# Performance work log

Measured on AMD Instinct MI355X. Metric: run time of the kernel, lower is better.

## Reference

```python
import jax, jax.numpy as jnp
import numpy as np

B, S, D, H = 2, 2048, 1024, 16
HD = D // H  # head_dim = 64


def _rope(t, cos, sin):
    # t: (B, H, S, HD); cos/sin: (S, HD//2) -> rotate interleaved pairs
    t2 = t.reshape(*t.shape[:-1], HD // 2, 2)
    t1, t2_ = t2[..., 0], t2[..., 1]
    c = cos[None, None, :, :]
    s = sin[None, None, :, :]
    out = jnp.stack([t1 * c - t2_ * s, t1 * s + t2_ * c], axis=-1)
    return out.reshape(t.shape)


def setup_inputs() -> dict:
    key = jax.random.key(0)
    ks = jax.random.split(key, 5)
    x = jax.random.normal(ks[0], (B, S, D), dtype=jnp.float32)
    attn_mask = jnp.tril(jnp.ones((S, S), dtype=bool))  # causal
    # standard RoPE angles: pos * inv_freq
    inv_freq = 1.0 / (10000.0 ** (jnp.arange(0, HD, 2, dtype=jnp.float32) / HD))
    freqs = jnp.arange(S, dtype=jnp.float32)[:, None] * inv_freq[None, :]  # (S, HD//2)
    std = 1.0 / np.sqrt(D)
    w_qkv = jax.random.normal(ks[1], (3 * D, D), dtype=jnp.float32) * std
    b_qkv = jnp.zeros((3 * D,), dtype=jnp.float32)
    w_proj = jax.random.normal(ks[2], (D, D), dtype=jnp.float32) * std
    b_proj = jnp.zeros((D,), dtype=jnp.float32)
    return {"x": x, "attn_mask": attn_mask, "freqs": freqs,
            "w_qkv": w_qkv, "b_qkv": b_qkv, "w_proj": w_proj, "b_proj": b_proj}


def reference(x, attn_mask, freqs, w_qkv, b_qkv, w_proj, b_proj):
    # QKV projection: (B,S,D) -> (B,S,3D), split per einops pattern (three, H, HD)
    qkv = x @ w_qkv.T + b_qkv
    qkv = qkv.reshape(B, S, 3, H, HD)
    q = jnp.transpose(qkv[:, :, 0], (0, 2, 1, 3))  # (B,H,S,HD)
    k = jnp.transpose(qkv[:, :, 1], (0, 2, 1, 3))
    v = jnp.transpose(qkv[:, :, 2], (0, 2, 1, 3))
    cos, sin = jnp.cos(freqs), jnp.sin(freqs)
    q = _rope(q, cos, sin)
    k = _rope(k, cos, sin)
    scale = 1.0 / np.sqrt(HD)
    scores = jnp.einsum("bhqd,bhkd->bhqk", q, k) * scale  # (B,H,S,S)
    scores = jnp.where(attn_mask[None, None, :, :], scores, jnp.finfo(scores.dtype).min)
    attn = jax.nn.softmax(scores, axis=-1)
    out = jnp.einsum("bhqk,bhkd->bhqd", attn, v)  # (B,H,S,HD)
    out = jnp.transpose(out, (0, 2, 1, 3)).reshape(B, S, D)
    return out @ w_proj.T + b_proj
```

## Files before the change

### kernel.cpp

```cpp
#include <hip/hip_runtime.h>

#define S_LEN 2048
#define NH 16
#define HD 64
#define DMODEL 1024

typedef __bf16 bf16x8 __attribute__((ext_vector_type(8)));
typedef float floatx4 __attribute__((ext_vector_type(4)));
typedef short short8 __attribute__((ext_vector_type(8)));

__device__ inline unsigned short f2bf(float f) {
    union { float f; unsigned u; } v; v.f = f;
    unsigned u = v.u;
    unsigned r = (u + 0x7FFFu + ((u >> 16) & 1u)) >> 16;
    return (unsigned short)r;
}

__device__ __forceinline__ void gload_lds16(const void* g, void* l) {
    __builtin_amdgcn_global_load_lds(
        (const __attribute__((address_space(1))) unsigned int*)g,
        (__attribute__((address_space(3))) unsigned int*)l, 16, 0, 0);
}

__device__ __forceinline__ void cvt4(const float4* __restrict__ src,
                                     uint2* __restrict__ dst, int i) {
    float4 v = src[i];
    union { unsigned short u[4]; uint2 d; } o;
    o.u[0] = f2bf(v.x); o.u[1] = f2bf(v.y); o.u[2] = f2bf(v.z); o.u[3] = f2bf(v.w);
    dst[i] = o.d;
}

__global__ __launch_bounds__(256) void prep_kernel(
    const float* __restrict__ x, const float* __restrict__ wq,
    const float* __restrict__ wp, const float* __restrict__ freqs,
    unsigned short* __restrict__ xb, unsigned short* __restrict__ wqb,
    unsigned short* __restrict__ wpb, float2* __restrict__ cs)
{
    const int tid = blockIdx.x * 256 + threadIdx.x;
    const int nth = gridDim.x * 256;
    for (int i = tid; i < (4096 * 1024) / 4; i += nth) cvt4((const float4*)x, (uint2*)xb, i);
    for (int i = tid; i < (3072 * 1024) / 4; i += nth) cvt4((const float4*)wq, (uint2*)wqb, i);
    for (int i = tid; i < (1024 * 1024) / 4; i += nth) cvt4((const float4*)wp, (uint2*)wpb, i);
    for (int i = tid; i < S_LEN * 32; i += nth) {
        const float f = freqs[i];
        float2 c; c.x = cosf(f); c.y = sinf(f);
        cs[i] = c;
    }
}

#define SROW(r) (((r) & 3) ^ (((r) >> 2) & 3))

#define QKV_STAGE(dA, dB, kk) do { \
    gload_lds16(ag + (kk),               (dA) + wv * 512); \
    gload_lds16(ag + 64 * DMODEL + (kk), (dA) + 2048 + wv * 512); \
    gload_lds16(bg + (kk),               (dB) + wv * 512); \
    gload_lds16(bg + 64 * DMODEL + (kk), (dB) + 2048 + wv * 512); \
} while (0)

#define QKV_COMPUTE(sA, sB) do { \
    bf16x8 af[4]; \
    _Pragma("unroll") for (int m_ = 0; m_ < 4; m_++) af[m_] = *(const bf16x8*)&(sA)[aoff[m_]]; \
    _Pragma("unroll") for (int n_ = 0; n_ < 4; n_++) { \
        bf16x8 bf = *(const bf16x8*)&(sB)[boff[n_]]; \
        _Pragma("unroll") for (int m_ = 0; m_ < 4; m_++) \
            acc[m_][n_] = __builtin_amdgcn_mfma_f32_16x16x32_bf16(af[m_], bf, acc[m_][n_], 0, 0, 0); \
    } \
} while (0)

__global__ __launch_bounds__(256, 3) void qkv_gemm_kernel(
    const unsigned short* __restrict__ xb, const unsigned short* __restrict__ wqb,
    const float* __restrict__ bias, const float2* __restrict__ cs,
    unsigned short* __restrict__ qb, unsigned short* __restrict__ kb,
    unsigned short* __restrict__ vb)
{
    __shared__ __align__(16) unsigned short smem[16384];
    unsigned short* A0 = smem;
    unsigned short* B0 = smem + 4096;
    unsigned short* A1 = smem + 8192;
    unsigned short* B1 = smem + 12288;

    const int t = threadIdx.x;
    const int v = (blockIdx.x & 7) * 96 + (blockIdx.x >> 3);
    const int mbase = (v / 24) * 128;
    const int nbase = (v % 24) * 128;
    const int wv = t >> 6, lane = t & 63;
    const int quad = lane >> 4, l16 = lane & 15;
    const int wr = wv >> 1, wc = wv & 1;

    floatx4 acc[4][4];
    #pragma unroll
    for (int m = 0; m < 4; m++)
        #pragma unroll
        for (int n = 0; n < 4; n++)
            #pragma unroll
            for (int r = 0; r < 4; r++) acc[m][n][r] = 0.f;

    const int srow = t >> 2;
    const int schunk = (t & 3) ^ SROW(srow);
    const unsigned short* ag = xb + (size_t)(mbase + srow) * DMODEL + schunk * 8;
    const unsigned short* bg = wqb + (size_t)(nbase + srow) * DMODEL + schunk * 8;

    const int Sl = SROW(l16);
    int aoff[4], boff[4];
    #pragma unroll
    for (int m = 0; m < 4; m++) aoff[m] = (wr * 64 + m * 16 + l16) * 32 + (quad ^ Sl) * 8;
    #pragma unroll
    for (int n = 0; n < 4; n++) boff[n] = (wc * 64 + n * 16 + l16) * 32 + (quad ^ Sl) * 8;

    QKV_STAGE(A0, B0, 0);
    __syncthreads();
    for (int k0 = 0; k0 < DMODEL; k0 += 64) {
        QKV_STAGE(A1, B1, k0 + 32);
        QKV_COMPUTE(A0, B0);
        __syncthreads();
        if (k0 + 64 < DMODEL) QKV_STAGE(A0, B0, k0 + 64);
        QKV_COMPUTE(A1, B1);
        __syncthreads();
    }

    const int part = nbase >> 10;
    const int bidx = mbase >> 11;
    const int s0   = mbase & 2047;

    if (part == 2) {
        unsigned short* Vt = smem;
        const int hb = (nbase & 1023) >> 6;
        float bvv[4];
        #pragma unroll
        for (int nt = 0; nt < 4; nt++) bvv[nt] = bias[nbase + wc * 64 + nt * 16 + l16];
        #pragma unroll
        for (int shalf = 0; shalf < 2; shalf++) {
            __syncthreads();
            if (wr == shalf) {
                #pragma unroll
                for (int nt = 0; nt < 4; nt++) {
                    const int hdl = wc * 64 + nt * 16 + l16;
                    #pragma unroll
                    for (int m = 0; m < 4; m++)
                        #pragma unroll
                        for (int r = 0; r < 4; r++)
                            Vt[hdl * 72 + m * 16 + quad * 4 + r] = f2bf(acc[m][nt][r] + bvv[nt]);
                }
            }
            __syncthreads();
            const int hdl = t & 127, sp = t >> 7;
            const size_t bh2 = (size_t)bidx * NH + hb + (hdl >> 6);
            #pragma unroll
            for (int c = 0; c < 4; c++) {
                const int sl0 = (sp * 4 + c) * 8;
                const int sg = s0 + shalf * 64 + sl0;
                short8 vv = *(const short8*)&Vt[hdl * 72 + sl0];
                *(short8*)&vb[((bh2 * 256 + (sg >> 3)) * 64 + (hdl & 63)) * 8] = vv;
            }
        }
    } else {
        const size_t bhb = (size_t)bidx * NH;
        const int odd = l16 & 1;
        #pragma unroll
        for (int nt = 0; nt < 4; nt++) {
            const int n_ = nbase + wc * 64 + nt * 16 + l16;
            const int hd = n_ & 63;
            const size_t bh = bhb + ((n_ & 1023) >> 6);
            const float bvv = bias[n_];
            const int ci = (nt * 16 + l16) >> 1;
            #pragma unroll
            for (int m = 0; m < 4; m++) {
                #pragma unroll
                for (int r = 0; r < 4; r++) {
                    const int s = s0 + wr * 64 + m * 16 + quad * 4 + r;
                    float val = acc[m][nt][r] + bvv;
                    float other = __shfl_xor(val, 1, 64);
                    const float2 csv = cs[(size_t)s * 32 + ci];
                    float outv = odd ? fmaf(other, csv.y, val * csv.x)
                                     : fmaf(-other, csv.y, val * csv.x);
                    if (part == 0) {
                        qb[(bh * S_LEN + s) * HD + hd] = f2bf(outv * 0.125f);
                    } else {
                        kb[((bh * 8 + (hd >> 3)) * (size_t)S_LEN + s) * 8 + (hd & 7)] = f2bf(outv);
                    }
                }
            }
        }
    }
}

__global__ __launch_bounds__(256, 4) void attn_kernel(
    const unsigned short* __restrict__ qb, const unsigned short* __restrict__ kb,
    const unsigned short* __restrict__ vbk, unsigned short* __restrict__ ao)
{
    __shared__ __align__(16) unsigned short Ks[8 * 512];
    __shared__ __align__(16) unsigned short Vt[8 * 512];
    __shared__ __align__(16) unsigned short Pw[4][16 * 72];

    const int t = threadIdx.x;
    const int wv = t >> 6, lane = t & 63, quad = lane >> 4, l16 = lane & 15;
    const int qt   = blockIdx.x >> 5;
    const int bhid = blockIdx.x & 31;
    const int h = bhid & 15, b = bhid >> 4;
    const size_t bh = (size_t)b * NH + h;
    const unsigned short* qg  = qb + bh * S_LEN * HD;
    const unsigned short* kgB = kb + bh * 8 * S_LEN * 8;
    const unsigned short* vgB = vbk + bh * 256 * 64 * 8;

    bf16x8 qf[2];
    {
        const unsigned short* q0 = qg + (size_t)(qt * 64 + wv * 16 + l16) * HD;
        qf[0] = *(const bf16x8*)&q0[quad * 8];
        qf[1] = *(const bf16x8*)&q0[32 + quad * 8];
    }

    bf16x8 ones;
    {
        union { short8 s; bf16x8 v; } o;
        for (int j = 0; j < 8; j++) o.s[j] = 0x3F80;
        ones = o.v;
    }

    floatx4 lfr = {0.f, 0.f, 0.f, 0.f};
    floatx4 Ofr[4];
    for (int nt = 0; nt < 4; nt++)
        for (int r = 0; r < 4; r++) Ofr[nt][r] = 0.f;

    const int ntiles = qt + 1;

    for (int kt = 0; kt < ntiles; kt++) {
        const int kbase = kt * 64;
        {
            const unsigned short* g0 = kgB + ((size_t)(2 * wv) * S_LEN + kbase + lane) * 8;
            gload_lds16(g0,             &Ks[(2 * wv) * 512]);
            gload_lds16(g0 + S_LEN * 8, &Ks[(2 * wv + 1) * 512]);
            const unsigned short* g1 = vgB + ((size_t)((kbase >> 3) + 2 * wv) * 64 + lane) * 8;
            gload_lds16(g1,          &Vt[(2 * wv) * 512]);
            gload_lds16(g1 + 64 * 8, &Vt[(2 * wv + 1) * 512]);
        }
        __syncthreads();

        float pex[4][4];
        #pragma unroll
        for (int sub = 0; sub < 4; sub++) {
            bf16x8 kf0 = *(const bf16x8*)&Ks[(0 * 4 + quad) * 512 + (sub * 16 + l16) * 8];
            bf16x8 kf1 = *(const bf16x8*)&Ks[(1 * 4 + quad) * 512 + (sub * 16 + l16) * 8];
            floatx4 sacc = {0.f, 0.f, 0.f, 0.f};
            sacc = __builtin_amdgcn_mfma_f32_16x16x32_bf16(kf0, qf[0], sacc, 0, 0, 0);
            sacc = __builtin_amdgcn_mfma_f32_16x16x32_bf16(kf1, qf[1], sacc, 0, 0, 0);
            #pragma unroll
            for (int r = 0; r < 4; r++) pex[sub][r] = sacc[r];
        }
        if (kt == qt) {
            const int q = qt * 64 + wv * 16 + l16;
            #pragma unroll
            for (int sub = 0; sub < 4; sub++)
                #pragma unroll
                for (int r = 0; r < 4; r++) {
                    const int key = kbase + sub * 16 + quad * 4 + r;
                    if (key > q) pex[sub][r] = -1e30f;
                }
        }
        #pragma unroll
        for (int sub = 0; sub < 4; sub++) {
            union { unsigned short s[4]; uint2 u; } pk;
            #pragma unroll
            for (int r = 0; r < 4; r++) pk.s[r] = f2bf(__expf(pex[sub][r]));
            *(uint2*)&Pw[wv][l16 * 72 + sub * 16 + quad * 4] = pk.u;
        }
        bf16x8 pf0 = *(const bf16x8*)&Pw[wv][l16 * 72 + quad * 8];
        bf16x8 pf1 = *(const bf16x8*)&Pw[wv][l16 * 72 + 32 + quad * 8];
        lfr = __builtin_amdgcn_mfma_f32_16x16x32_bf16(ones, pf0, lfr, 0, 0, 0);
        lfr = __builtin_amdgcn_mfma_f32_16x16x32_bf16(ones, pf1, lfr, 0, 0, 0);
        #pragma unroll
        for (int nt = 0; nt < 4; nt++) {
            bf16x8 v0 = *(const bf16x8*)&Vt[(0 * 4 + quad) * 512 + (nt * 16 + l16) * 8];
            bf16x8 v1 = *(const bf16x8*)&Vt[(1 * 4 + quad) * 512 + (nt * 16 + l16) * 8];
            Ofr[nt] = __builtin_amdgcn_mfma_f32_16x16x32_bf16(pf0, v0, Ofr[nt], 0, 0, 0);
            Ofr[nt] = __builtin_amdgcn_mfma_f32_16x16x32_bf16(pf1, v1, Ofr[nt], 0, 0, 0);
        }
        __syncthreads();
    }

    float linv[4];
    #pragma unroll
    for (int r = 0; r < 4; r++) {
        float lq = __shfl(lfr[0], (lane & 48) | (quad * 4 + r), 64);
        linv[r] = 1.f / lq;
    }
    #pragma unroll
    for (int nt = 0; nt < 4; nt++)
        #pragma unroll
        for (int r = 0; r < 4; r++) {
            const int s = qt * 64 + wv * 16 + quad * 4 + r;
            ao[((size_t)b * S_LEN + s) * DMODEL + h * HD + nt * 16 + l16] =
                f2bf(Ofr[nt][r] * linv[r]);
        }
}

#define PROJ_STAGE(dA, dB, kk) do { \
    gload_lds16(ag + (kk),               (dA) + wv * 512); \
    gload_lds16(ag + 64 * DMODEL + (kk), (dA) + 2048 + wv * 512); \
    gload_lds16(bg + (kk),               (dB) + wv * 512); \
} while (0)

#define PROJ_COMPUTE(sA, sB) do { \
    bf16x8 af[4]; \
    _Pragma("unroll") for (int m_ = 0; m_ < 4; m_++) af[m_] = *(const bf16x8*)&(sA)[aoff[m_]]; \
    _Pragma("unroll") for (int n_ = 0; n_ < 2; n_++) { \
        bf16x8 bf = *(const bf16x8*)&(sB)[boff[n_]]; \
        _Pragma("unroll") for (int m_ = 0; m_ < 4; m_++) \
            acc[m_][n_] = __builtin_amdgcn_mfma_f32_16x16x32_bf16(af[m_], bf, acc[m_][n_], 0, 0, 0); \
    } \
} while (0)

__global__ __launch_bounds__(256, 3) void proj_kernel(
    const unsigned short* __restrict__ a, const unsigned short* __restrict__ wpb,
    const float* __restrict__ bias, float* __restrict__ out)
{
    __shared__ __align__(16) unsigned short smem[12288];
    unsigned short* A0 = smem;
    unsigned short* B0 = smem + 4096;
    unsigned short* A1 = smem + 6144;
    unsigned short* B1 = smem + 10240;

    const int t = threadIdx.x;
    const int v = (blockIdx.x & 7) * 64 + (blockIdx.x >> 3);
    const int mbase = (v >> 4) * 128;
    const int nbase = (v & 15) * 64;
    const int wv = t >> 6, lane = t & 63, quad = lane >> 4, l16 = lane & 15;
    const int wr = wv >> 1, wc = wv & 1;

    floatx4 acc[4][2];
    #pragma unroll
    for (int m = 0; m < 4; m++)
        #pragma unroll
        for (int n = 0; n < 2; n++)
            #pragma unroll
            for (int r = 0; r < 4; r++) acc[m][n][r] = 0.f;

    const int srow = t >> 2;
    const int schunk = (t & 3) ^ SROW(srow);
    const unsigned short* ag = a + (size_t)(mbase + srow) * DMODEL + schunk * 8;
    const unsigned short* bg = wpb + (size_t)(nbase + srow) * DMODEL + schunk * 8;

    const int Sl = SROW(l16);
    int aoff[4], boff[2];
    #pragma unroll
    for (int m = 0; m < 4; m++) aoff[m] = (wr * 64 + m * 16 + l16) * 32 + (quad ^ Sl) * 8;
    #pragma unroll
    for (int n = 0; n < 2; n++) boff[n] = (wc * 32 + n * 16 + l16) * 32 + (quad ^ Sl) * 8;

    PROJ_STAGE(A0, B0, 0);
    __syncthreads();
    for (int k0 = 0; k0 < DMODEL; k0 += 64) {
        PROJ_STAGE(A1, B1, k0 + 32);
        PROJ_COMPUTE(A0, B0);
        __syncthreads();
        if (k0 + 64 < DMODEL) PROJ_STAGE(A0, B0, k0 + 64);
        PROJ_COMPUTE(A1, B1);
        __syncthreads();
    }

    #pragma unroll
    for (int n = 0; n < 2; n++) {
        const int nn = nbase + wc * 32 + n * 16 + l16;
        const float bvv = bias[nn];
        #pragma unroll
        for (int m = 0; m < 4; m++)
            #pragma unroll
            for (int r = 0; r < 4; r++)
                out[(size_t)(mbase + wr * 64 + m * 16 + quad * 4 + r) * DMODEL + nn] =
                    acc[m][n][r] + bvv;
    }
}

extern "C" void kernel_launch(void* const* d_in, const int* in_sizes, int n_in,
                              void* d_out, int out_size, void* d_ws, size_t ws_size,
                              hipStream_t stream) {
    const float* x      = (const float*)d_in[0];
    const float* freqs  = (const float*)d_in[2];
    const float* w_qkv  = (const float*)d_in[3];
    const float* b_qkv  = (const float*)d_in[4];
    const float* w_proj = (const float*)d_in[5];
    const float* b_proj = (const float*)d_in[6];
    float* out = (float*)d_out;

    unsigned short* ws = (unsigned short*)d_ws;
    const size_t HSZ = (size_t)2 * NH * S_LEN * HD;
    unsigned short* qb  = ws;
    unsigned short* kb  = ws + HSZ;
    unsigned short* vb  = ws + 2 * HSZ;
    unsigned short* ao  = ws + 3 * HSZ;
    unsigned short* xb  = ws + 4 * HSZ;
    unsigned short* wqb = xb + (size_t)4096 * 1024;
    unsigned short* wpb = wqb + (size_t)3072 * 1024;
    float2* cs = (float2*)(wpb + (size_t)1024 * 1024);

    prep_kernel<<<2048, 256, 0, stream>>>(x, w_qkv, w_proj, freqs, xb, wqb, wpb, cs);
    qkv_gemm_kernel<<<768, 256, 0, stream>>>(xb, wqb, b_qkv, cs, qb, kb, vb);
    attn_kernel<<<1024, 256, 0, stream>>>(qb, kb, vb, ao);
    proj_kernel<<<512, 256, 0, stream>>>(ao, wpb, b_proj, out);
}
```

Baseline: 200.2 us.

## Double-buffer K/V tiles in attention and schedule heavy causal tiles first

The attention kernel now keeps two LDS buffers for K and V, so the global-to-LDS load of the next key tile is issued while the current tile is being computed. This hides load latency behind compute. Query tiles are also launched in reverse order, so the longest causal rows start first and the tail of the grid is better balanced. Launch bounds drop from 4 to 3 blocks per SM because the doubled LDS footprint reduces occupancy.

```diff
diff --git a/kernel.cpp b/kernel.cpp
--- a/kernel.cpp
+++ b/kernel.cpp
@@ -184,17 +184,17 @@
     }
 }
 
-__global__ __launch_bounds__(256, 4) void attn_kernel(
+__global__ __launch_bounds__(256, 3) void attn_kernel(
     const unsigned short* __restrict__ qb, const unsigned short* __restrict__ kb,
     const unsigned short* __restrict__ vbk, unsigned short* __restrict__ ao)
 {
-    __shared__ __align__(16) unsigned short Ks[8 * 512];
-    __shared__ __align__(16) unsigned short Vt[8 * 512];
+    __shared__ __align__(16) unsigned short Ks[2][8 * 512];
+    __shared__ __align__(16) unsigned short Vt[2][8 * 512];
     __shared__ __align__(16) unsigned short Pw[4][16 * 72];
 
     const int t = threadIdx.x;
     const int wv = t >> 6, lane = t & 63, quad = lane >> 4, l16 = lane & 15;
-    const int qt   = blockIdx.x >> 5;
+    const int qt   = 31 - (blockIdx.x >> 5);
     const int bhid = blockIdx.x & 31;
     const int h = bhid & 15, b = bhid >> 4;
     const size_t bh = (size_t)b * NH + h;
@@ -223,57 +223,66 @@
 
     const int ntiles = qt + 1;
 
-    for (int kt = 0; kt < ntiles; kt++) {
-        const int kbase = kt * 64;
-        {
-            const unsigned short* g0 = kgB + ((size_t)(2 * wv) * S_LEN + kbase + lane) * 8;
-            gload_lds16(g0,             &Ks[(2 * wv) * 512]);
-            gload_lds16(g0 + S_LEN * 8, &Ks[(2 * wv + 1) * 512]);
-            const unsigned short* g1 = vgB + ((size_t)((kbase >> 3) + 2 * wv) * 64 + lane) * 8;
-            gload_lds16(g1,          &Vt[(2 * wv) * 512]);
-            gload_lds16(g1 + 64 * 8, &Vt[(2 * wv + 1) * 512]);
-        }
-        __syncthreads();
-
-        float pex[4][4];
-        #pragma unroll
-        for (int sub = 0; sub < 4; sub++) {
-            bf16x8 kf0 = *(const bf16x8*)&Ks[(0 * 4 + quad) * 512 + (sub * 16 + l16) * 8];
-            bf16x8 kf1 = *(const bf16x8*)&Ks[(1 * 4 + quad) * 512 + (sub * 16 + l16) * 8];
-            floatx4 sacc = {0.f, 0.f, 0.f, 0.f};
-            sacc = __builtin_amdgcn_mfma_f32_16x16x32_bf16(kf0, qf[0], sacc, 0, 0, 0);
-            sacc = __builtin_amdgcn_mfma_f32_16x16x32_bf16(kf1, qf[1], sacc, 0, 0, 0);
-            #pragma unroll
-            for (int r = 0; r < 4; r++) pex[sub][r] = sacc[r];
-        }
-        if (kt == qt) {
-            const int q = qt * 64 + wv * 16 + l16;
-            #pragma unroll
-            for (int sub = 0; sub < 4; sub++)
-                #pragma unroll
-                for (int r = 0; r < 4; r++) {
-                    const int key = kbase + sub * 16 + quad * 4 + r;
-                    if (key > q) pex[sub][r] = -1e30f;
-                }
-        }
-        #pragma unroll
-        for (int sub = 0; sub < 4; sub++) {
-            union { unsigned short s[4]; uint2 u; } pk;
-            #pragma unroll
-            for (int r = 0; r < 4; r++) pk.s[r] = f2bf(__expf(pex[sub][r]));
-            *(uint2*)&Pw[wv][l16 * 72 + sub * 16 + quad * 4] = pk.u;
-        }
-        bf16x8 pf0 = *(const bf16x8*)&Pw[wv][l16 * 72 + quad * 8];
-        bf16x8 pf1 = *(const bf16x8*)&Pw[wv][l16 * 72 + 32 + quad * 8];
-        lfr = __builtin_amdgcn_mfma_f32_16x16x32_bf16(ones, pf0, lfr, 0, 0, 0);
-        lfr = __builtin_amdgcn_mfma_f32_16x16x32_bf16(ones, pf1, lfr, 0, 0, 0);
-        #pragma unroll
-        for (int nt = 0; nt < 4; nt++) {
-            bf16x8 v0 = *(const bf16x8*)&Vt[(0 * 4 + quad) * 512 + (nt * 16 + l16) * 8];
-            bf16x8 v1 = *(const bf16x8*)&Vt[(1 * 4 + quad) * 512 + (nt * 16 + l16) * 8];
-            Ofr[nt] = __builtin_amdgcn_mfma_f32_16x16x32_bf16(pf0, v0, Ofr[nt], 0, 0, 0);
-            Ofr[nt] = __builtin_amdgcn_mfma_f32_16x16x32_bf16(pf1, v1, Ofr[nt], 0, 0, 0);
-        }
+#define ATTN_STAGE(bufi, kt_) do { \
+    const int kb_ = (kt_) * 64; \
+    const unsigned short* g0 = kgB + ((size_t)(2 * wv) * S_LEN + kb_ + lane) * 8; \
+    gload_lds16(g0,             &Ks[bufi][(2 * wv) * 512]); \
+    gload_lds16(g0 + S_LEN * 8, &Ks[bufi][(2 * wv + 1) * 512]); \
+    const unsigned short* g1 = vgB + ((size_t)((kb_ >> 3) + 2 * wv) * 64 + lane) * 8; \
+    gload_lds16(g1,          &Vt[bufi][(2 * wv) * 512]); \
+    gload_lds16(g1 + 64 * 8, &Vt[bufi][(2 * wv + 1) * 512]); \
+} while (0)
+
+#define ATTN_COMPUTE(bufi, kt_) do { \
+    const int kbase = (kt_) * 64; \
+    float pex[4][4]; \
+    _Pragma("unroll") for (int sub = 0; sub < 4; sub++) { \
+        bf16x8 kf0 = *(const bf16x8*)&Ks[bufi][(0 * 4 + quad) * 512 + (sub * 16 + l16) * 8]; \
+        bf16x8 kf1 = *(const bf16x8*)&Ks[bufi][(1 * 4 + quad) * 512 + (sub * 16 + l16) * 8]; \
+        floatx4 sacc = {0.f, 0.f, 0.f, 0.f}; \
+        sacc = __builtin_amdgcn_mfma_f32_16x16x32_bf16(kf0, qf[0], sacc, 0, 0, 0); \
+        sacc = __builtin_amdgcn_mfma_f32_16x16x32_bf16(kf1, qf[1], sacc, 0, 0, 0); \
+        _Pragma("unroll") for (int r = 0; r < 4; r++) pex[sub][r] = sacc[r]; \
+    } \
+    if ((kt_) == qt) { \
+        const int q = qt * 64 + wv * 16 + l16; \
+        _Pragma("unroll") for (int sub = 0; sub < 4; sub++) \
+            _Pragma("unroll") for (int r = 0; r < 4; r++) { \
+                const int key = kbase + sub * 16 + quad * 4 + r; \
+                if (key > q) pex[sub][r] = -1e30f; \
+            } \
+    } \
+    _Pragma("unroll") for (int sub = 0; sub < 4; sub++) { \
+        union { unsigned short s[4]; uint2 u; } pk; \
+        _Pragma("unroll") for (int r = 0; r < 4; r++) pk.s[r] = f2bf(__expf(pex[sub][r])); \
+        *(uint2*)&Pw[wv][l16 * 72 + sub * 16 + quad * 4] = pk.u; \
+    } \
+    { \
+        bf16x8 pf0 = *(const bf16x8*)&Pw[wv][l16 * 72 + quad * 8]; \
+        bf16x8 pf1 = *(const bf16x8*)&Pw[wv][l16 * 72 + 32 + quad * 8]; \
+        lfr = __builtin_amdgcn_mfma_f32_16x16x32_bf16(ones, pf0, lfr, 0, 0, 0); \
+        lfr = __builtin_amdgcn_mfma_f32_16x16x32_bf16(ones, pf1, lfr, 0, 0, 0); \
+        _Pragma("unroll") for (int nt = 0; nt < 4; nt++) { \
+            bf16x8 v0 = *(const bf16x8*)&Vt[bufi][(0 * 4 + quad) * 512 + (nt * 16 + l16) * 8]; \
+            bf16x8 v1 = *(const bf16x8*)&Vt[bufi][(1 * 4 + quad) * 512 + (nt * 16 + l16) * 8]; \
+            Ofr[nt] = __builtin_amdgcn_mfma_f32_16x16x32_bf16(pf0, v0, Ofr[nt], 0, 0, 0); \
+            Ofr[nt] = __builtin_amdgcn_mfma_f32_16x16x32_bf16(pf1, v1, Ofr[nt], 0, 0, 0); \
+        } \
+    } \
+} while (0)
+
+    ATTN_STAGE(0, 0);
+    __syncthreads();
+    for (int kt = 0; kt < ntiles; ) {
+        if (kt + 1 < ntiles) ATTN_STAGE(1, kt + 1);
+        ATTN_COMPUTE(0, kt);
+        kt++;
+        if (kt >= ntiles) break;
+        __syncthreads();
+        if (kt + 1 < ntiles) ATTN_STAGE(0, kt + 1);
+        ATTN_COMPUTE(1, kt);
+        kt++;
+        if (kt >= ntiles) break;
         __syncthreads();
     }
 
@@ -291,6 +300,8 @@
             ao[((size_t)b * S_LEN + s) * DMODEL + h * HD + nt * 16 + l16] =
                 f2bf(Ofr[nt][r] * linv[r]);
         }
+#undef ATTN_STAGE
+#undef ATTN_COMPUTE
 }
 
 #define PROJ_STAGE(dA, dB, kk) do { \
```

New measurement: 192.3 us. 1.04x faster.
